# Kernel tuning notes

Hardware: AMD Instinct MI355X
Metric: run time of the kernel (lower is better)

Reference implementation:

```python
import jax, jax.numpy as jnp
import numpy as np

B, S, E, H, DK, DV = 2, 2048, 1024, 16, 64, 64
NEG = -1e9


def setup_inputs() -> dict:
    key = jax.random.key(0)
    ks = jax.random.split(key, 12)
    s = 0.02
    return {
        "query": jax.random.normal(ks[0], (B, S, E), jnp.float32),
        "key": jax.random.normal(ks[1], (B, S, E), jnp.float32),
        "value": jax.random.normal(ks[2], (B, S, E), jnp.float32),
        "mask": jax.random.randint(ks[3], (B, S, S), 0, 2, jnp.int32),
        "Wq": jax.random.normal(ks[4], (E, H * DK), jnp.float32) * s,
        "bq": jnp.zeros((H * DK,), jnp.float32),
        "Wk": jax.random.normal(ks[5], (E, H * DK), jnp.float32) * s,
        "bk": jnp.zeros((H * DK,), jnp.float32),
        "Wv": jax.random.normal(ks[6], (E, H * DV), jnp.float32) * s,
        "bv": jnp.zeros((H * DV,), jnp.float32),
        "Wo": jax.random.normal(ks[7], (H * DV, E), jnp.float32) * s,
        "bo": jnp.zeros((E,), jnp.float32),
    }


def reference(query, key, value, mask, Wq, bq, Wk, bk, Wv, bv, Wo, bo):
    # projections, then split heads: (B,S,H*D) -> (B,H,S,D)
    q = (query @ Wq + bq).reshape(B, S, H, DK).transpose(0, 2, 1, 3)
    k = (key @ Wk + bk).reshape(B, S, H, DK).transpose(0, 2, 1, 3)
    v = (value @ Wv + bv).reshape(B, S, H, DV).transpose(0, 2, 1, 3)
    scores = jnp.einsum("bhqd,bhkd->bhqk", q, k) / jnp.sqrt(jnp.float32(DK))
    scores = jnp.where(mask[:, None, :, :] == 0, jnp.float32(NEG), scores)
    weights = jax.nn.softmax(scores, axis=-1)
    ctx = jnp.einsum("bhqk,bhkd->bhqd", weights, v)
    ctx = ctx.transpose(0, 2, 1, 3).reshape(B, S, H * DV)
    return ctx @ Wo + bo
```

## Files before the change

kernel.cpp:

```cpp
#include <hip/hip_runtime.h>

typedef __attribute__((ext_vector_type(8))) short s16x8;
typedef __attribute__((ext_vector_type(4))) float f32x4;
typedef __attribute__((ext_vector_type(16))) float f32x16;
typedef unsigned short u16;
typedef unsigned int u32;
typedef unsigned long long u64;

__device__ __forceinline__ u16 f2bf(float f) {
  u32 u = __builtin_bit_cast(u32, f);
  u += 0x7fff + ((u >> 16) & 1);
  return (u16)(u >> 16);
}

__device__ __forceinline__ float exp2fast(float x) {
#if __has_builtin(__builtin_amdgcn_exp2f)
  return __builtin_amdgcn_exp2f(x);
#else
  return __expf(x * 0.6931471805599453f);
#endif
}

__device__ __forceinline__ void gload16(const void* g, void* l) {
  __builtin_amdgcn_global_load_lds((const __attribute__((address_space(1))) u32*)g,
                                   (__attribute__((address_space(3))) u32*)l, 16, 0, 0);
}

#define MFMA(a, b, c) __builtin_amdgcn_mfma_f32_16x16x32_bf16((a), (b), (c), 0, 0, 0)
#define MFMA32(a, b, c) __builtin_amdgcn_mfma_f32_32x32x16_bf16((a), (b), (c), 0, 0, 0)

#define QSCALE 0.18033688011112042f

__global__ __launch_bounds__(256) void prep(
    const float* __restrict__ q, const float* __restrict__ k, const float* __restrict__ v,
    u16* __restrict__ oq, u16* __restrict__ ok, u16* __restrict__ ov,
    const float* __restrict__ W0, const float* __restrict__ W1,
    const float* __restrict__ W2, const float* __restrict__ W3,
    u16* __restrict__ T0, u16* __restrict__ T1, u16* __restrict__ T2, u16* __restrict__ T3,
    const int* __restrict__ mask, u64* __restrict__ mb) {
  __shared__ float t[32][33];
  const int bx = blockIdx.x, tid = threadIdx.x;
  if (bx < 6144) {
    int z = bx >> 11;
    const float* src = (z == 0) ? q : (z == 1) ? k : v;
    u16* dst = (z == 0) ? oq : (z == 1) ? ok : ov;
    int i = (bx & 2047) * 256 + tid;
    const float4* s4 = (const float4*)src;
    float4 a = s4[2 * i], bb = s4[2 * i + 1];
    uint4 o;
    o.x = (u32)f2bf(a.x) | ((u32)f2bf(a.y) << 16);
    o.y = (u32)f2bf(a.z) | ((u32)f2bf(a.w) << 16);
    o.z = (u32)f2bf(bb.x) | ((u32)f2bf(bb.y) << 16);
    o.w = (u32)f2bf(bb.z) | ((u32)f2bf(bb.w) << 16);
    ((uint4*)dst)[i] = o;
  } else if (bx < 10240) {
    int r = bx - 6144;
    int z = r >> 10, t2 = r & 1023;
    const float* W = (z == 0) ? W0 : (z == 1) ? W1 : (z == 2) ? W2 : W3;
    u16* WT = (z == 0) ? T0 : (z == 1) ? T1 : (z == 2) ? T2 : T3;
    int nb = t2 & 31, kb = t2 >> 5;
    int tx = tid & 31, ty = tid >> 5;
    int n = nb * 32 + tx;
#pragma unroll
    for (int j = 0; j < 4; j++) {
      int kk = kb * 32 + ty + 8 * j;
      t[ty + 8 * j][tx] = W[(size_t)kk * 1024 + n];
    }
    __syncthreads();
    int kk = kb * 32 + tx;
#pragma unroll
    for (int j = 0; j < 4; j++) {
      int n2 = nb * 32 + ty + 8 * j;
      WT[(size_t)n2 * 1024 + kk] = f2bf(t[tx][ty + 8 * j]);
    }
  } else {
    int wi = (bx - 10240) * 4 + (tid >> 6);
    int lane = tid & 63;
    u64 bits = __ballot(mask[((size_t)wi << 6) + lane] != 0);
    if (lane == 0) {
      int b_ = wi >> 16, q_ = (wi >> 5) & 2047, t_ = wi & 31;
      mb[((size_t)b_ << 16) + ((size_t)t_ << 11) + q_] = bits;
    }
  }
}

template <int BM, int BN>
__device__ __forceinline__ void gemm_core(const u16* __restrict__ A, const u16* __restrict__ BT,
                                          int m0, int n0, u16* Ash, u16* Bsh,
                                          f32x4 (&acc)[BM / 32][BN / 32]) {
  constexpr int MF = BM / 32, NF = BN / 32;
  constexpr int BATCH = BM / 32 + BN / 32;
  const int tid = threadIdx.x;
  const int lane = tid & 63, wid = tid >> 6;
  const int r16 = lane & 15, g = lane >> 4;
  const int wm = wid >> 1, wn = wid & 1;
  const int swz = r16 & 7;
  const f32x4 vz = {0.f, 0.f, 0.f, 0.f};
#pragma unroll
  for (int mf = 0; mf < MF; mf++)
#pragma unroll
    for (int nf = 0; nf < NF; nf++) acc[mf][nf] = vz;

  auto stage = [&](int buf, int k0) {
#pragma unroll
    for (int i = 0; i < MF; i++) {
      int ch = i * 256 + tid;
      int row = ch >> 3, sc = (ch & 7) ^ (row & 7);
      gload16(A + (((size_t)(m0 + row)) << 10) + k0 + sc * 8,
              Ash + (size_t)buf * (BM * 64) + ch * 8);
    }
#pragma unroll
    for (int i = 0; i < NF; i++) {
      int ch = i * 256 + tid;
      int row = ch >> 3, sc = (ch & 7) ^ (row & 7);
      gload16(BT + (((size_t)(n0 + row)) << 10) + k0 + sc * 8,
              Bsh + (size_t)buf * (BN * 64) + ch * 8);
    }
  };

  asm volatile("" ::: "memory");
  stage(0, 0);
  asm volatile("" ::: "memory");
  stage(1, 64);
  asm volatile("" ::: "memory");

  for (int t = 0; t < 16; t++) {
    const int cur = t & 1;
    if (t == 15) {
      asm volatile("s_waitcnt vmcnt(0)" ::: "memory");
    } else if constexpr (BATCH == 8) {
      asm volatile("s_waitcnt vmcnt(8)" ::: "memory");
    } else {
      asm volatile("s_waitcnt vmcnt(6)" ::: "memory");
    }
    asm volatile("s_barrier" ::: "memory");

    const u16* Acur = Ash + (size_t)cur * (BM * 64);
    const u16* Bcur = Bsh + (size_t)cur * (BN * 64);
    __builtin_amdgcn_s_setprio(1);
#pragma unroll
    for (int kk = 0; kk < 2; kk++) {
      const int c = (kk * 4 + g);
      s16x8 af[MF], bfr[NF];
#pragma unroll
      for (int mf = 0; mf < MF; mf++)
        af[mf] = *(const s16x8*)(Acur + ((wm * (BM / 2) + mf * 16 + r16) << 6) +
                                 ((c ^ swz) << 3));
#pragma unroll
      for (int nf = 0; nf < NF; nf++)
        bfr[nf] = *(const s16x8*)(Bcur + ((wn * (BN / 2) + nf * 16 + r16) << 6) +
                                  ((c ^ swz) << 3));
#pragma unroll
      for (int mf = 0; mf < MF; mf++)
#pragma unroll
        for (int nf = 0; nf < NF; nf++) acc[mf][nf] = MFMA(af[mf], bfr[nf], acc[mf][nf]);
    }
    __builtin_amdgcn_s_setprio(0);

    asm volatile("s_barrier" ::: "memory");
    if (t + 2 < 16) stage(cur, (t + 2) * 64);
  }
}

__global__ __launch_bounds__(256, 3) void proj_gemm(
    const u16* __restrict__ Xq, const u16* __restrict__ Xk, const u16* __restrict__ Xv,
    const u16* __restrict__ WqT, const u16* __restrict__ WkT, const u16* __restrict__ WvT,
    const float* __restrict__ bq, const float* __restrict__ bk, const float* __restrict__ bv,
    u16* __restrict__ Qo, u16* __restrict__ Ko, u16* __restrict__ Vto) {
  __shared__ u16 Ash[2 * 64 * 64], Bsh[2 * 128 * 64];
  const int z = blockIdx.z;
  const u16* A = (z == 0) ? Xq : (z == 1) ? Xk : Xv;
  const u16* BT = (z == 0) ? WqT : (z == 1) ? WkT : WvT;
  const float* bias = (z == 0) ? bq : (z == 1) ? bk : bv;
  u16* O = (z == 0) ? Qo : (z == 1) ? Ko : Vto;
  const float sc = (z == 0) ? QSCALE : 1.0f;
  int lin = blockIdx.x + ((int)blockIdx.y << 3);
  int work = (lin & 7) * 64 + (lin >> 3);
  const int m0 = (work >> 3) * 64, n0 = (work & 7) * 128;
  f32x4 acc[2][4];
  gemm_core<64, 128>(A, BT, m0, n0, Ash, Bsh, acc);
  const int tid = threadIdx.x, lane = tid & 63, wid = tid >> 6;
  const int r16 = lane & 15, g = lane >> 4, wm = wid >> 1, wn = wid & 1;
#pragma unroll
  for (int nf = 0; nf < 4; nf++) {
    int col = n0 + wn * 64 + nf * 16 + r16;
    float bb = bias[col];
    int h = col >> 6, d = col & 63;
#pragma unroll
    for (int mf = 0; mf < 2; mf++) {
#pragma unroll
      for (int ri = 0; ri < 4; ri++) {
        int row = m0 + wm * 32 + mf * 16 + g * 4 + ri;
        int b_ = row >> 11, s_ = row & 2047;
        u16 val = f2bf((acc[mf][nf][ri] + bb) * sc);
        if (z < 2)
          O[((((size_t)b_ * 16 + h) * 2048 + s_) << 6) + d] = val;
        else
          O[((((size_t)b_ * 16 + h) * 64 + d) << 11) + s_] = val;
      }
    }
  }
}

__global__ __launch_bounds__(256, 3) void out_gemm(const u16* __restrict__ ctx,
                                                   const u16* __restrict__ WoT,
                                                   const float* __restrict__ bo,
                                                   float* __restrict__ out) {
  __shared__ u16 Ash[2 * 64 * 64], Bsh[2 * 128 * 64];
  int lin = blockIdx.x + ((int)blockIdx.y << 3);
  int work = (lin & 7) * 64 + (lin >> 3);
  const int m0 = (work >> 3) * 64, n0 = (work & 7) * 128;
  f32x4 acc[2][4];
  gemm_core<64, 128>(ctx, WoT, m0, n0, Ash, Bsh, acc);
  const int tid = threadIdx.x, lane = tid & 63, wid = tid >> 6;
  const int r16 = lane & 15, g = lane >> 4, wm = wid >> 1, wn = wid & 1;
#pragma unroll
  for (int nf = 0; nf < 4; nf++) {
    int col = n0 + wn * 64 + nf * 16 + r16;
    float bb = bo[col];
#pragma unroll
    for (int mf = 0; mf < 2; mf++) {
#pragma unroll
      for (int ri = 0; ri < 4; ri++) {
        int row = m0 + wm * 32 + mf * 16 + g * 4 + ri;
        out[((size_t)row << 10) + col] = acc[mf][nf][ri] + bb;
      }
    }
  }
}

__device__ __forceinline__ s16x8 pack4u(u32 a0, u32 a1, u32 b0, u32 b1) {
  union { u32 u[4]; s16x8 v; } p;
  p.u[0] = a0; p.u[1] = a1; p.u[2] = b0; p.u[3] = b1;
  return p.v;
}

__device__ __forceinline__ void softpack(const f32x16& sv, u32 wm, s16x8& pA, s16x8& pB) {
  float e[16];
#pragma unroll
  for (int qd = 0; qd < 4; qd++)
#pragma unroll
    for (int j = 0; j < 4; j++) {
      const int bit = qd * 8 + j;
      float ex = exp2fast(sv[qd * 4 + j]);
      u32 sext = (u32)(((int)(wm << (31 - bit))) >> 31);
      e[qd * 4 + j] = __builtin_bit_cast(float, __builtin_bit_cast(u32, ex) & sext);
    }
#pragma unroll
  for (int n = 0; n < 2; n++) {
    u32 a0, a1, b0, b1;
    asm("v_cvt_pk_bf16_f32 %0, %1, %2" : "=v"(a0) : "v"(e[n * 8 + 0]), "v"(e[n * 8 + 1]));
    asm("v_cvt_pk_bf16_f32 %0, %1, %2" : "=v"(a1) : "v"(e[n * 8 + 2]), "v"(e[n * 8 + 3]));
    asm("v_cvt_pk_bf16_f32 %0, %1, %2" : "=v"(b0) : "v"(e[n * 8 + 4]), "v"(e[n * 8 + 5]));
    asm("v_cvt_pk_bf16_f32 %0, %1, %2" : "=v"(b1) : "v"(e[n * 8 + 6]), "v"(e[n * 8 + 7]));
    asm("v_permlane32_swap_b32 %0, %1" : "+v"(a0), "+v"(b0));
    asm("v_permlane32_swap_b32 %0, %1" : "+v"(a1), "+v"(b1));
    if (n == 0) pA = pack4u(a0, a1, b0, b1);
    else        pB = pack4u(a0, a1, b0, b1);
  }
}

__global__ __launch_bounds__(256, 2) void flash_attn(const u16* __restrict__ Q,
                                                     const u16* __restrict__ K,
                                                     const u16* __restrict__ Vt,
                                                     const u64* __restrict__ Mb64,
                                                     u16* __restrict__ ctx) {
  __shared__ __align__(16) u16 Ksh[4][64][64];
  __shared__ __align__(16) u16 Vsh[4][64][64];

  const int tid = threadIdx.x, w = tid >> 6, lane = tid & 63;
  const int l31 = lane & 31, h5 = lane >> 5, l7 = lane & 7;

  int work = ((int)blockIdx.x & 7) * 64 + ((int)blockIdx.x >> 3);
  const int qt = work & 15, bh = work >> 4;
  const int b = bh >> 4, h = bh & 15;
  const int q0 = qt * 128 + w * 32;

  const u16* Qb = Q + ((size_t)bh << 17);
  const u16* Kb = K + ((size_t)bh << 17);
  const u16* Vb = Vt + ((size_t)bh << 17);
  const u64* MrowT = Mb64 + ((size_t)b << 16) + (q0 + l31);

  const int srow = tid >> 3, sk16 = tid & 7;
#define STAGE(buf, kv0)                                                                   \
  {                                                                                       \
    _Pragma("unroll") for (int i = 0; i < 2; i++) {                                       \
      int row = i * 32 + srow;                                                            \
      int sc = sk16 ^ (row & 7);                                                          \
      gload16(Kb + (((size_t)((kv0) + row)) << 6) + sc * 8,                               \
              (char*)&Ksh[buf][0][0] + (i * 256 + tid) * 16);                             \
      gload16(Vb + (((size_t)row) << 11) + (kv0) + sc * 8,                                \
              (char*)&Vsh[buf][0][0] + (i * 256 + tid) * 16);                             \
    }                                                                                     \
  }

  s16x8 aq[4];
#pragma unroll
  for (int dk = 0; dk < 4; dk++)
    aq[dk] = *(const s16x8*)(Qb + ((q0 + l31) << 6) + dk * 16 + h5 * 8);
  asm volatile("" ::: "memory");
  STAGE(0, 0);
  STAGE(1, 64);
  u64 m_c0 = MrowT[0], m_c1 = MrowT[(size_t)1 << 11];
  asm volatile("" ::: "memory");
  STAGE(2, 128);
  STAGE(3, 192);
  u64 m_n0 = MrowT[(size_t)2 << 11], m_n1 = MrowT[(size_t)3 << 11];
  asm volatile("" ::: "memory");

  s16x8 vones;
#pragma unroll
  for (int j = 0; j < 8; j++) vones[j] = (short)0x3F80;

  f32x16 o0, o1, o4;
#pragma unroll
  for (int r = 0; r < 16; r++) { o0[r] = 0.f; o1[r] = 0.f; o4[r] = 0.f; }

  for (int t = 0; t < 16; t++) {
    const int base = (t & 1) * 2;
    if (t == 15) {
      asm volatile("s_waitcnt vmcnt(0)" ::: "memory");
    } else {
      asm volatile("s_waitcnt vmcnt(10)" ::: "memory");
    }
    asm volatile("s_barrier" ::: "memory");

    const u16* KcA = &Ksh[base][0][0];
    const u16* KcB = &Ksh[base + 1][0][0];
    const u16* VcA = &Vsh[base][0][0];
    const u16* VcB = &Vsh[base + 1][0][0];

    f32x16 s0, s1, s2, s3;
#pragma unroll
    for (int r = 0; r < 16; r++) { s0[r] = 0.f; s1[r] = 0.f; s2[r] = 0.f; s3[r] = 0.f; }
    __builtin_amdgcn_s_setprio(1);
#pragma unroll
    for (int dk = 0; dk < 4; dk++) {
      int ch = (((dk << 1) + h5) ^ l7) << 3;
      s16x8 akA0 = *(const s16x8*)(KcA + (l31 << 6) + ch);
      s16x8 akA1 = *(const s16x8*)(KcA + ((32 + l31) << 6) + ch);
      s16x8 akB0 = *(const s16x8*)(KcB + (l31 << 6) + ch);
      s16x8 akB1 = *(const s16x8*)(KcB + ((32 + l31) << 6) + ch);
      s0 = MFMA32(akA0, aq[dk], s0);
      s1 = MFMA32(akA1, aq[dk], s1);
      s2 = MFMA32(akB0, aq[dk], s2);
      s3 = MFMA32(akB1, aq[dk], s3);
    }
    __builtin_amdgcn_s_setprio(0);

    u64 mshA = m_c0 >> (h5 << 2);
    s16x8 pa[4];
    softpack(s0, (u32)mshA, pa[0], pa[1]);
    softpack(s1, (u32)(mshA >> 32), pa[2], pa[3]);
    __builtin_amdgcn_s_setprio(1);
#pragma unroll
    for (int km = 0; km < 4; km++) {
      int ch = (((km << 1) + h5) ^ l7) << 3;
      s16x8 bv0 = *(const s16x8*)(VcA + (l31 << 6) + ch);
      s16x8 bv1 = *(const s16x8*)(VcA + ((32 + l31) << 6) + ch);
      o0 = MFMA32(pa[km], bv0, o0);
      o1 = MFMA32(pa[km], bv1, o1);
      o4 = MFMA32(pa[km], vones, o4);
    }
    __builtin_amdgcn_s_setprio(0);

    u64 mshB = m_c1 >> (h5 << 2);
    s16x8 pb[4];
    softpack(s2, (u32)mshB, pb[0], pb[1]);
    softpack(s3, (u32)(mshB >> 32), pb[2], pb[3]);
    __builtin_amdgcn_s_setprio(1);
#pragma unroll
    for (int km = 0; km < 4; km++) {
      int ch = (((km << 1) + h5) ^ l7) << 3;
      s16x8 bv0 = *(const s16x8*)(VcB + (l31 << 6) + ch);
      s16x8 bv1 = *(const s16x8*)(VcB + ((32 + l31) << 6) + ch);
      o0 = MFMA32(pb[km], bv0, o0);
      o1 = MFMA32(pb[km], bv1, o1);
      o4 = MFMA32(pb[km], vones, o4);
    }
    __builtin_amdgcn_s_setprio(0);

    asm volatile("s_barrier" ::: "memory");
    u64 mw0 = 0, mw1 = 0;
    if (t + 2 < 16) {
      STAGE(base, (2 * t + 4) * 64);
      STAGE(base + 1, (2 * t + 5) * 64);
      mw0 = MrowT[(size_t)(2 * t + 4) << 11];
      mw1 = MrowT[(size_t)(2 * t + 5) << 11];
    }
    m_c0 = m_n0; m_c1 = m_n1;
    m_n0 = mw0;  m_n1 = mw1;
  }
#undef STAGE

#pragma unroll
  for (int r = 0; r < 16; r++) {
    int qr = (r & 3) + 8 * (r >> 2) + 4 * h5;
    size_t rowoff = ((size_t)((b << 11) + q0 + qr)) << 10;
    float iv = 1.f / o4[r];
    ctx[rowoff + (h << 6) + l31]      = f2bf(o0[r] * iv);
    ctx[rowoff + (h << 6) + 32 + l31] = f2bf(o1[r] * iv);
  }
}

extern "C" void kernel_launch(void* const* d_in, const int* in_sizes, int n_in,
                              void* d_out, int out_size, void* d_ws, size_t ws_size,
                              hipStream_t stream) {
  const float* query = (const float*)d_in[0];
  const float* key_  = (const float*)d_in[1];
  const float* value = (const float*)d_in[2];
  const int*   mask  = (const int*)d_in[3];
  const float* Wq = (const float*)d_in[4];
  const float* bq = (const float*)d_in[5];
  const float* Wk = (const float*)d_in[6];
  const float* bk = (const float*)d_in[7];
  const float* Wv = (const float*)d_in[8];
  const float* bv = (const float*)d_in[9];
  const float* Wo = (const float*)d_in[10];
  const float* bo = (const float*)d_in[11];

  const size_t MB = 1048576;
  char* ws = (char*)d_ws;
  u16* Xq  = (u16*)(ws + 0 * MB);
  u16* Xk  = (u16*)(ws + 8 * MB);
  u16* Xv  = (u16*)(ws + 16 * MB);
  u16* WqT = (u16*)(ws + 24 * MB);
  u16* WkT = (u16*)(ws + 26 * MB);
  u16* WvT = (u16*)(ws + 28 * MB);
  u16* WoT = (u16*)(ws + 30 * MB);
  u16* Qd  = (u16*)(ws + 32 * MB);
  u16* Kd  = (u16*)(ws + 40 * MB);
  u16* Vtd = (u16*)(ws + 48 * MB);
  u16* ctx = (u16*)(ws + 56 * MB);
  u64* Mb  = (u64*)(ws + 72 * MB);

  prep<<<43008, 256, 0, stream>>>(query, key_, value, Xq, Xk, Xv,
                                  Wq, Wk, Wv, Wo, WqT, WkT, WvT, WoT, mask, Mb);

  proj_gemm<<<dim3(8, 64, 3), 256, 0, stream>>>(Xq, Xk, Xv, WqT, WkT, WvT, bq, bk, bv,
                                                Qd, Kd, Vtd);
  flash_attn<<<512, 256, 0, stream>>>(Qd, Kd, Vtd, Mb, ctx);
  out_gemm<<<dim3(8, 64), 256, 0, stream>>>(ctx, WoT, bo, (float*)d_out);
}
```

Measured before the change: 141.3 us.

## Fuse fp32-to-bf16 input conversion into projection GEMM A-tile loading

Removes the separate prep pass that converted query/key/value from fp32 to bf16 in workspace. The projection GEMM now loads fp32 A rows directly into registers, packs them to bf16 with v_cvt_pk_bf16_f32, and writes them into swizzled LDS, while B tiles still go through async global-to-LDS loads. This avoids writing and re-reading 24MB of intermediate bf16 data. In exchange, A loads are no longer async to LDS, register pressure rises, and each block reads twice the bytes for A.

Measured after the change: 145.6 us. 3.1% more time.

```diff
diff --git a/kernel.cpp b/kernel.cpp
--- a/kernel.cpp
+++ b/kernel.cpp
@@ -32,30 +32,14 @@
 #define QSCALE 0.18033688011112042f
 
 __global__ __launch_bounds__(256) void prep(
-    const float* __restrict__ q, const float* __restrict__ k, const float* __restrict__ v,
-    u16* __restrict__ oq, u16* __restrict__ ok, u16* __restrict__ ov,
     const float* __restrict__ W0, const float* __restrict__ W1,
     const float* __restrict__ W2, const float* __restrict__ W3,
     u16* __restrict__ T0, u16* __restrict__ T1, u16* __restrict__ T2, u16* __restrict__ T3,
     const int* __restrict__ mask, u64* __restrict__ mb) {
   __shared__ float t[32][33];
   const int bx = blockIdx.x, tid = threadIdx.x;
-  if (bx < 6144) {
-    int z = bx >> 11;
-    const float* src = (z == 0) ? q : (z == 1) ? k : v;
-    u16* dst = (z == 0) ? oq : (z == 1) ? ok : ov;
-    int i = (bx & 2047) * 256 + tid;
-    const float4* s4 = (const float4*)src;
-    float4 a = s4[2 * i], bb = s4[2 * i + 1];
-    uint4 o;
-    o.x = (u32)f2bf(a.x) | ((u32)f2bf(a.y) << 16);
-    o.y = (u32)f2bf(a.z) | ((u32)f2bf(a.w) << 16);
-    o.z = (u32)f2bf(bb.x) | ((u32)f2bf(bb.y) << 16);
-    o.w = (u32)f2bf(bb.z) | ((u32)f2bf(bb.w) << 16);
-    ((uint4*)dst)[i] = o;
-  } else if (bx < 10240) {
-    int r = bx - 6144;
-    int z = r >> 10, t2 = r & 1023;
+  if (bx < 4096) {
+    int z = bx >> 10, t2 = bx & 1023;
     const float* W = (z == 0) ? W0 : (z == 1) ? W1 : (z == 2) ? W2 : W3;
     u16* WT = (z == 0) ? T0 : (z == 1) ? T1 : (z == 2) ? T2 : T3;
     int nb = t2 & 31, kb = t2 >> 5;
@@ -74,7 +58,7 @@
       WT[(size_t)n2 * 1024 + kk] = f2bf(t[tx][ty + 8 * j]);
     }
   } else {
-    int wi = (bx - 10240) * 4 + (tid >> 6);
+    int wi = (bx - 4096) * 4 + (tid >> 6);
     int lane = tid & 63;
     u64 bits = __ballot(mask[((size_t)wi << 6) + lane] != 0);
     if (lane == 0) {
@@ -163,13 +147,15 @@
 }
 
 __global__ __launch_bounds__(256, 3) void proj_gemm(
-    const u16* __restrict__ Xq, const u16* __restrict__ Xk, const u16* __restrict__ Xv,
+    const float* __restrict__ Xq32, const float* __restrict__ Xk32,
+    const float* __restrict__ Xv32,
     const u16* __restrict__ WqT, const u16* __restrict__ WkT, const u16* __restrict__ WvT,
     const float* __restrict__ bq, const float* __restrict__ bk, const float* __restrict__ bv,
     u16* __restrict__ Qo, u16* __restrict__ Ko, u16* __restrict__ Vto) {
-  __shared__ u16 Ash[2 * 64 * 64], Bsh[2 * 128 * 64];
+  __shared__ u16 Ash[2 * 64 * 64];
+  __shared__ u16 Bsh[2 * 128 * 64];
   const int z = blockIdx.z;
-  const u16* A = (z == 0) ? Xq : (z == 1) ? Xk : Xv;
+  const float* A32 = (z == 0) ? Xq32 : (z == 1) ? Xk32 : Xv32;
   const u16* BT = (z == 0) ? WqT : (z == 1) ? WkT : WvT;
   const float* bias = (z == 0) ? bq : (z == 1) ? bk : bv;
   u16* O = (z == 0) ? Qo : (z == 1) ? Ko : Vto;
@@ -177,10 +163,109 @@
   int lin = blockIdx.x + ((int)blockIdx.y << 3);
   int work = (lin & 7) * 64 + (lin >> 3);
   const int m0 = (work >> 3) * 64, n0 = (work & 7) * 128;
+
+  const int tid = threadIdx.x;
+  const int lane = tid & 63, wid = tid >> 6;
+  const int r16 = lane & 15, g = lane >> 4;
+  const int wm = wid >> 1, wn = wid & 1;
+  const int swz = r16 & 7;
+  const int arow = tid >> 2, aq4 = tid & 3;
+  const float* Asrc = A32 + (size_t)(m0 + arow) * 1024 + aq4 * 16;
+  u16* AwBase = Ash + arow * 64;
+
+  auto stageB = [&](int buf, int k0) {
+#pragma unroll
+    for (int i = 0; i < 4; i++) {
+      int ch = i * 256 + tid;
+      int row = ch >> 3, scc = (ch & 7) ^ (row & 7);
+      gload16(BT + (((size_t)(n0 + row)) << 10) + k0 + scc * 8,
+              Bsh + (size_t)buf * 8192 + ch * 8);
+    }
+  };
+  auto writeA = [&](int buf, const float4* v) {
+    u32 p[8];
+#pragma unroll
+    for (int j = 0; j < 4; j++) {
+      asm("v_cvt_pk_bf16_f32 %0, %1, %2" : "=v"(p[2 * j]) : "v"(v[j].x), "v"(v[j].y));
+      asm("v_cvt_pk_bf16_f32 %0, %1, %2" : "=v"(p[2 * j + 1]) : "v"(v[j].z), "v"(v[j].w));
+    }
+    u16* base = AwBase + buf * 4096;
+    uint4 lo; lo.x = p[0]; lo.y = p[1]; lo.z = p[2]; lo.w = p[3];
+    uint4 hi; hi.x = p[4]; hi.y = p[5]; hi.z = p[6]; hi.w = p[7];
+    *(uint4*)(base + (((2 * aq4) ^ (arow & 7)) << 3)) = lo;
+    *(uint4*)(base + (((2 * aq4 + 1) ^ (arow & 7)) << 3)) = hi;
+  };
+
   f32x4 acc[2][4];
-  gemm_core<64, 128>(A, BT, m0, n0, Ash, Bsh, acc);
-  const int tid = threadIdx.x, lane = tid & 63, wid = tid >> 6;
-  const int r16 = lane & 15, g = lane >> 4, wm = wid >> 1, wn = wid & 1;
+  const f32x4 vz = {0.f, 0.f, 0.f, 0.f};
+#pragma unroll
+  for (int mf = 0; mf < 2; mf++)
+#pragma unroll
+    for (int nf = 0; nf < 4; nf++) acc[mf][nf] = vz;
+
+  float4 t0[4], ahold[4];
+  asm volatile("" ::: "memory");
+#pragma unroll
+  for (int j = 0; j < 4; j++) t0[j] = *(const float4*)(Asrc + j * 4);
+  asm volatile("" ::: "memory");
+  stageB(0, 0);
+  asm volatile("" ::: "memory");
+#pragma unroll
+  for (int j = 0; j < 4; j++) ahold[j] = *(const float4*)(Asrc + 64 + j * 4);
+  asm volatile("" ::: "memory");
+  stageB(1, 64);
+  asm volatile("" ::: "memory");
+  writeA(0, t0);
+  asm volatile("" ::: "memory");
+
+  for (int t = 0; t < 16; t++) {
+    const int cur = t & 1;
+    if (t == 15) {
+      asm volatile("s_waitcnt vmcnt(0) lgkmcnt(0)" ::: "memory");
+    } else {
+      asm volatile("s_waitcnt vmcnt(8) lgkmcnt(0)" ::: "memory");
+    }
+    asm volatile("s_barrier" ::: "memory");
+
+    const u16* Acur = Ash + (size_t)cur * 4096;
+    const u16* Bcur = Bsh + (size_t)cur * 8192;
+    __builtin_amdgcn_s_setprio(1);
+#pragma unroll
+    for (int kk = 0; kk < 2; kk++) {
+      const int c = (kk * 4 + g);
+      s16x8 af[2], bfr[4];
+#pragma unroll
+      for (int mf = 0; mf < 2; mf++)
+        af[mf] = *(const s16x8*)(Acur + ((wm * 32 + mf * 16 + r16) << 6) + ((c ^ swz) << 3));
+#pragma unroll
+      for (int nf = 0; nf < 4; nf++)
+        bfr[nf] = *(const s16x8*)(Bcur + ((wn * 64 + nf * 16 + r16) << 6) + ((c ^ swz) << 3));
+#pragma unroll
+      for (int mf = 0; mf < 2; mf++)
+#pragma unroll
+        for (int nf = 0; nf < 4; nf++) acc[mf][nf] = MFMA(af[mf], bfr[nf], acc[mf][nf]);
+    }
+    __builtin_amdgcn_s_setprio(0);
+
+    asm volatile("s_barrier" ::: "memory");
+    if (t + 2 < 16) {
+      float4 tn[4];
+      asm volatile("" ::: "memory");
+#pragma unroll
+      for (int j = 0; j < 4; j++) tn[j] = *(const float4*)(Asrc + (t + 2) * 64 + j * 4);
+      asm volatile("" ::: "memory");
+      stageB(cur, (t + 2) * 64);
+      asm volatile("" ::: "memory");
+      writeA(cur ^ 1, ahold);
+      asm volatile("" ::: "memory");
+#pragma unroll
+      for (int j = 0; j < 4; j++) ahold[j] = tn[j];
+    } else if (t + 1 < 16) {
+      writeA(cur ^ 1, ahold);
+      asm volatile("" ::: "memory");
+    }
+  }
+
 #pragma unroll
   for (int nf = 0; nf < 4; nf++) {
     int col = n0 + wn * 64 + nf * 16 + r16;
@@ -421,9 +506,6 @@
 
   const size_t MB = 1048576;
   char* ws = (char*)d_ws;
-  u16* Xq  = (u16*)(ws + 0 * MB);
-  u16* Xk  = (u16*)(ws + 8 * MB);
-  u16* Xv  = (u16*)(ws + 16 * MB);
   u16* WqT = (u16*)(ws + 24 * MB);
   u16* WkT = (u16*)(ws + 26 * MB);
   u16* WvT = (u16*)(ws + 28 * MB);
@@ -434,11 +516,10 @@
   u16* ctx = (u16*)(ws + 56 * MB);
   u64* Mb  = (u64*)(ws + 72 * MB);
 
-  prep<<<43008, 256, 0, stream>>>(query, key_, value, Xq, Xk, Xv,
-                                  Wq, Wk, Wv, Wo, WqT, WkT, WvT, WoT, mask, Mb);
-
-  proj_gemm<<<dim3(8, 64, 3), 256, 0, stream>>>(Xq, Xk, Xv, WqT, WkT, WvT, bq, bk, bv,
-                                                Qd, Kd, Vtd);
+  prep<<<36864, 256, 0, stream>>>(Wq, Wk, Wv, Wo, WqT, WkT, WvT, WoT, mask, Mb);
+
+  proj_gemm<<<dim3(8, 64, 3), 256, 0, stream>>>(query, key_, value, WqT, WkT, WvT,
+                                                bq, bk, bv, Qd, Kd, Vtd);
   flash_attn<<<512, 256, 0, stream>>>(Qd, Kd, Vtd, Mb, ctx);
   out_gemm<<<dim3(8, 64), 256, 0, stream>>>(ctx, WoT, bo, (float*)d_out);
 }
```
